# Performance work log

Hardware: AMD Instinct MI355X
Metric: run time of the kernel (lower is better)

Reference implementation:

```python
import jax, jax.numpy as jnp
import numpy as np

N = 50000   # nodes
E = 800000  # edges (avg degree 16)
C = 96      # in = hidden = out channels


def setup_inputs() -> dict:
    key = jax.random.key(0)
    ks = jax.random.split(key, 8)
    s = np.float32(1.0 / np.sqrt(C))
    x = jax.random.normal(ks[0], (N, C), dtype=jnp.float32)
    edge_index = jax.random.randint(ks[1], (2, E), 0, N, dtype=jnp.int64)
    W1 = jax.random.normal(ks[2], (C, C), dtype=jnp.float32) * s
    Wr1 = jax.random.normal(ks[3], (C, C), dtype=jnp.float32) * s
    b1 = jnp.zeros((C,), dtype=jnp.float32)
    W2 = jax.random.normal(ks[4], (C, C), dtype=jnp.float32) * s
    Wr2 = jax.random.normal(ks[5], (C, C), dtype=jnp.float32) * s
    b2 = jnp.zeros((C,), dtype=jnp.float32)
    return {"x": x, "edge_index": edge_index,
            "W1": W1, "Wr1": Wr1, "b1": b1,
            "W2": W2, "Wr2": Wr2, "b2": b2}


def spline_conv(x, edge_index, W, W_root, b):
    """Gather-transform-scatter message passing (SplineConv core, mean aggr)."""
    src, dst = edge_index[0], edge_index[1]
    h = x @ W                                   # [N, C] transform once per node
    msg = h[src]                                # [E, C] edge gather
    agg = jax.ops.segment_sum(msg, dst, num_segments=N)        # scatter-add
    deg = jax.ops.segment_sum(jnp.ones((E,), x.dtype), dst, num_segments=N)
    agg = agg / jnp.maximum(deg, 1.0)[:, None]  # mean aggregation
    return agg + x @ W_root + b                 # root weight + bias


def reference(x, edge_index, W1, Wr1, b1, W2, Wr2, b2):
    h = jax.nn.relu(spline_conv(x, edge_index, W1, Wr1, b1))
    out = spline_conv(h, edge_index, W2, Wr2, b2)
    return out.reshape(-1)  # generalization of x.view(1600)
```

## Files before the change

### kernel.cpp

```cpp
#include <hip/hip_runtime.h>

#define C 96
#define BKT_SHIFT 9
#define BKT_SIZE 512
#define CAP 10240
#define EB 2048
typedef unsigned char u8;
typedef unsigned short u16;
typedef unsigned int u32;
typedef __attribute__((ext_vector_type(8))) short short8;
typedef __attribute__((ext_vector_type(4))) float floatx4;
typedef __attribute__((ext_vector_type(2))) float floatx2;

__device__ inline u16 f2bf(float f) {
    union { float f; u32 u; } v; v.f = f;
    u32 r = v.u + 0x7fff + ((v.u >> 16) & 1);
    return (u16)(r >> 16);
}
__device__ inline u32 pk4_fp8(float a, float b, float c, float d) {
    u32 w = 0;
    w = __builtin_amdgcn_cvt_pk_fp8_f32(a, b, w, false);
    w = __builtin_amdgcn_cvt_pk_fp8_f32(c, d, w, true);
    return w;
}
__device__ inline u8 f2fp8(float a) {
    return (u8)(__builtin_amdgcn_cvt_pk_fp8_f32(a, a, 0, false) & 0xff);
}

__global__ __launch_bounds__(256) void binA_kernel(const int* __restrict__ src,
                                                   const int* __restrict__ dst,
                                                   int* __restrict__ blk_cnt,
                                                   int* __restrict__ blk_off,
                                                   u32* __restrict__ stage, int E) {
    __shared__ u32 s_word[EB];
    __shared__ int s_cnt[128];
    __shared__ int s_inc[128];
    int bid = blockIdx.x;
    int t = threadIdx.x;
    int e0 = bid * EB;
    int cnt_here = min(EB, E - e0);

    for (int i = t; i < 128; i += 256) s_cnt[i] = 0;
    __syncthreads();

    int my_src[EB / 256], my_dl[EB / 256], my_b[EB / 256], my_rank[EB / 256];
    int nmine = 0;
#pragma unroll
    for (int k = 0; k < EB / 256; k++) {
        int i = t + k * 256;
        if (i < cnt_here) {
            int s = src[e0 + i], d = dst[e0 + i];
            int b = d >> BKT_SHIFT;
            my_src[nmine] = s;
            my_dl[nmine] = d & (BKT_SIZE - 1);
            my_b[nmine] = b;
            my_rank[nmine] = atomicAdd(&s_cnt[b], 1);
            nmine++;
        }
    }
    __syncthreads();

    if (t < 128) s_inc[t] = s_cnt[t];
    __syncthreads();
    for (int off = 1; off < 128; off <<= 1) {
        int x2 = (t >= off && t < 128) ? s_inc[t - off] : 0;
        __syncthreads();
        if (t < 128) s_inc[t] += x2;
        __syncthreads();
    }
    if (t < 128) {
        blk_cnt[bid * 128 + t] = s_cnt[t];
        blk_off[bid * 128 + t] = s_inc[t] - s_cnt[t];
    }

    for (int k = 0; k < nmine; k++) {
        int b = my_b[k];
        int slot = (s_inc[b] - s_cnt[b]) + my_rank[k];
        s_word[slot] = ((u32)my_dl[k] << 16) | (u32)my_src[k];
    }
    __syncthreads();

    for (int i = t; i < cnt_here; i += 256) stage[(size_t)bid * EB + i] = s_word[i];
}

__global__ __launch_bounds__(256) void binB_kernel(const u32* __restrict__ stage,
                                                   const int* __restrict__ blk_cnt,
                                                   const int* __restrict__ blk_off,
                                                   int* __restrict__ deg,
                                                   int* __restrict__ row_off,
                                                   u16* __restrict__ csr, int N, int DB,
                                                   int nbkt,
                                                   const float* __restrict__ x,
                                                   u16* __restrict__ xb,
                                                   u8* __restrict__ xf8, int n16, int CX,
                                                   const float* W0, const float* W1,
                                                   const float* W2, const float* W3,
                                                   u16* T0, u16* T1, u16* T2, u16* T3) {
    int bid = blockIdx.x;
    int t = threadIdx.x;
    if (bid >= nbkt) {
        if (bid < nbkt + CX) {
            int i = (bid - nbkt) * 256 + t;
            if (i >= n16) return;
            const float4* p = (const float4*)x + (size_t)i * 4;
            float4 a = p[0], b = p[1], c = p[2], d = p[3];
            short8 o0, o1;
            o0[0] = (short)f2bf(a.x); o0[1] = (short)f2bf(a.y);
            o0[2] = (short)f2bf(a.z); o0[3] = (short)f2bf(a.w);
            o0[4] = (short)f2bf(b.x); o0[5] = (short)f2bf(b.y);
            o0[6] = (short)f2bf(b.z); o0[7] = (short)f2bf(b.w);
            o1[0] = (short)f2bf(c.x); o1[1] = (short)f2bf(c.y);
            o1[2] = (short)f2bf(c.z); o1[3] = (short)f2bf(c.w);
            o1[4] = (short)f2bf(d.x); o1[5] = (short)f2bf(d.y);
            o1[6] = (short)f2bf(d.z); o1[7] = (short)f2bf(d.w);
            *(short8*)(xb + (size_t)i * 16) = o0;
            *(short8*)(xb + (size_t)i * 16 + 8) = o1;
            uint4 f8;
            f8.x = pk4_fp8(a.x, a.y, a.z, a.w);
            f8.y = pk4_fp8(b.x, b.y, b.z, b.w);
            f8.z = pk4_fp8(c.x, c.y, c.z, c.w);
            f8.w = pk4_fp8(d.x, d.y, d.z, d.w);
            *(uint4*)(xf8 + (size_t)i * 16) = f8;
        } else {
            int w = bid - nbkt - CX;
            const float* W = w == 0 ? W0 : w == 1 ? W1 : w == 2 ? W2 : W3;
            u16* T = w == 0 ? T0 : w == 1 ? T1 : w == 2 ? T2 : T3;
            for (int i = t; i < C * C; i += 256) {
                int k = i / C, n = i - k * C;
                T[n * C + k] = f2bf(W[i]);
            }
        }
        return;
    }

    __shared__ int cnt[BKT_SIZE];
    __shared__ int cur[BKT_SIZE];
    __shared__ int ssum[256];
    int b = bid;
    int n0 = b << BKT_SHIFT;
    int nn = min(BKT_SIZE, N - n0);
    int s0 = b * CAP;

    for (int i = t; i < BKT_SIZE; i += 256) cnt[i] = 0;
    __syncthreads();

    for (int i = t; i < DB; i += 256) {
        int len = blk_cnt[i * 128 + b];
        const u32* run = stage + (size_t)i * EB + blk_off[i * 128 + b];
        for (int j = 0; j < len; j++) atomicAdd(&cnt[run[j] >> 16], 1);
    }
    __syncthreads();

    int a0 = cnt[2 * t], a1 = cnt[2 * t + 1];
    ssum[t] = a0 + a1;
    __syncthreads();
    for (int off = 1; off < 256; off <<= 1) {
        int x2 = (t >= off) ? ssum[t - off] : 0;
        __syncthreads();
        ssum[t] += x2;
        __syncthreads();
    }
    int excl = ssum[t] - (a0 + a1);
    if (2 * t < nn) { deg[n0 + 2 * t] = a0; row_off[n0 + 2 * t] = s0 + excl; }
    if (2 * t + 1 < nn) { deg[n0 + 2 * t + 1] = a1; row_off[n0 + 2 * t + 1] = s0 + excl + a0; }
    __syncthreads();
    cur[2 * t] = s0 + excl;
    cur[2 * t + 1] = s0 + excl + a0;
    __syncthreads();

    for (int i = t; i < DB; i += 256) {
        int len = blk_cnt[i * 128 + b];
        const u32* run = stage + (size_t)i * EB + blk_off[i * 128 + b];
        for (int j = 0; j < len; j++) {
            u32 w = run[j];
            int p = atomicAdd(&cur[w >> 16], 1);
            csr[p] = (u16)(w & 0xffffu);
        }
    }
}

template <bool RELU, bool WF8, typename OT>
__global__ __launch_bounds__(256, 4) void layer_kernel(const u16* __restrict__ Xbf,
                                                       const u8* __restrict__ Xf8,
                                                       const int* __restrict__ row_off,
                                                       const int* __restrict__ deg,
                                                       const u16* __restrict__ csr,
                                                       const u16* __restrict__ WTA,
                                                       const u16* __restrict__ WTR,
                                                       const float* __restrict__ BIAS,
                                                       OT* __restrict__ Y,
                                                       u8* __restrict__ Yf8, int n) {
    __shared__ u16 sA[64 * 104];
    __shared__ int s_dg[64];
    __shared__ int s_perm[64];
    const int t = threadIdx.x;
    const int row0 = blockIdx.x * 64;

    if (t < 64) {
        int node = row0 + t;
        s_dg[t] = (node < n) ? deg[node] : 0;
    }
    __syncthreads();
    if (t < 64) {
        int di = s_dg[t];
        int r = 0;
#pragma unroll 8
        for (int j = 0; j < 64; j++) {
            int dj = s_dg[j];
            r += (dj < di) || (dj == di && j < t);
        }
        s_perm[r] = t;
    }
    __syncthreads();

    {
        int nl = s_perm[t >> 2];
        int node = row0 + nl;
        int q = t & 3;
        float acc[24];
#pragma unroll
        for (int i = 0; i < 24; i++) acc[i] = 0.f;
        int d = 0, start = 0;
        if (node < n) { start = row_off[node]; d = s_dg[nl]; }
        const int off4 = q * 16;
        const int off2 = 64 + q * 8;

        int j = 0;
        if (d >= 4) {
            int si[4];
#pragma unroll
            for (int k = 0; k < 4; k++) si[k] = csr[start + k];
            for (; j + 8 <= d; j += 4) {
                uint4 va[4];
                uint2 vb[4];
#pragma unroll
                for (int k = 0; k < 4; k++) {
                    const u8* p = Xf8 + (size_t)si[k] * 96;
                    va[k] = *(const uint4*)(p + off4);
                    vb[k] = *(const uint2*)(p + off2);
                }
                int sn[4];
#pragma unroll
                for (int k = 0; k < 4; k++) sn[k] = csr[start + j + 4 + k];
#pragma unroll
                for (int k = 0; k < 4; k++) {
                    u32 ws[6] = {va[k].x, va[k].y, va[k].z,
                                 va[k].w, vb[k].x, vb[k].y};
#pragma unroll
                    for (int i = 0; i < 6; i++) {
                        floatx2 lo = __builtin_amdgcn_cvt_pk_f32_fp8(ws[i], false);
                        floatx2 hi = __builtin_amdgcn_cvt_pk_f32_fp8(ws[i], true);
                        acc[4 * i]     += lo[0];
                        acc[4 * i + 1] += lo[1];
                        acc[4 * i + 2] += hi[0];
                        acc[4 * i + 3] += hi[1];
                    }
                }
#pragma unroll
                for (int k = 0; k < 4; k++) si[k] = sn[k];
            }
            {
                uint4 va[4];
                uint2 vb[4];
#pragma unroll
                for (int k = 0; k < 4; k++) {
                    const u8* p = Xf8 + (size_t)si[k] * 96;
                    va[k] = *(const uint4*)(p + off4);
                    vb[k] = *(const uint2*)(p + off2);
                }
#pragma unroll
                for (int k = 0; k < 4; k++) {
                    u32 ws[6] = {va[k].x, va[k].y, va[k].z,
                                 va[k].w, vb[k].x, vb[k].y};
#pragma unroll
                    for (int i = 0; i < 6; i++) {
                        floatx2 lo = __builtin_amdgcn_cvt_pk_f32_fp8(ws[i], false);
                        floatx2 hi = __builtin_amdgcn_cvt_pk_f32_fp8(ws[i], true);
                        acc[4 * i]     += lo[0];
                        acc[4 * i + 1] += lo[1];
                        acc[4 * i + 2] += hi[0];
                        acc[4 * i + 3] += hi[1];
                    }
                }
                j += 4;
            }
        }
        for (; j < d; j++) {
            const u8* p = Xf8 + (size_t)csr[start + j] * 96;
            uint4 va = *(const uint4*)(p + off4);
            uint2 vb = *(const uint2*)(p + off2);
            u32 ws[6] = {va.x, va.y, va.z, va.w, vb.x, vb.y};
#pragma unroll
            for (int i = 0; i < 6; i++) {
                floatx2 lo = __builtin_amdgcn_cvt_pk_f32_fp8(ws[i], false);
                floatx2 hi = __builtin_amdgcn_cvt_pk_f32_fp8(ws[i], true);
                acc[4 * i]     += lo[0];
                acc[4 * i + 1] += lo[1];
                acc[4 * i + 2] += hi[0];
                acc[4 * i + 3] += hi[1];
            }
        }
        float inv = 1.0f / fmaxf((float)d, 1.0f);
        u16* dl = sA + nl * 104;
        short8 o0, o1, o2;
#pragma unroll
        for (int i = 0; i < 8; i++) {
            o0[i] = (short)f2bf(acc[i] * inv);
            o1[i] = (short)f2bf(acc[8 + i] * inv);
            o2[i] = (short)f2bf(acc[16 + i] * inv);
        }
        *(short8*)(dl + q * 16) = o0;
        *(short8*)(dl + q * 16 + 8) = o1;
        *(short8*)(dl + 64 + q * 8) = o2;
    }
    __syncthreads();

    const int lane = t & 63;
    const int w = t >> 6;
    const int quad = lane >> 4;
    const int l16 = lane & 15;
    const int r0 = row0 + w * 16;

    floatx4 acc6[6];
#pragma unroll
    for (int i = 0; i < 6; i++) acc6[i] = (floatx4){0.f, 0.f, 0.f, 0.f};

    {
        const u16* Ap = sA + (w * 16 + l16) * 104 + quad * 8;
        const u16* Wp = WTA + l16 * C + quad * 8;
#pragma unroll
        for (int ks = 0; ks < 3; ks++) {
            short8 a = *(const short8*)(Ap + ks * 32);
#pragma unroll
            for (int nt = 0; nt < 6; nt++) {
                short8 b = *(const short8*)(Wp + nt * 16 * C + ks * 32);
                acc6[nt] = __builtin_amdgcn_mfma_f32_16x16x32_bf16(a, b, acc6[nt], 0, 0, 0);
            }
        }
    }
    {
        int arow = r0 + l16;
        if (arow >= n) arow = n - 1;
        const u16* Xp = Xbf + (size_t)arow * C + quad * 8;
        const u16* Wp = WTR + l16 * C + quad * 8;
#pragma unroll
        for (int ks = 0; ks < 3; ks++) {
            short8 a = *(const short8*)(Xp + ks * 32);
#pragma unroll
            for (int nt = 0; nt < 6; nt++) {
                short8 b = *(const short8*)(Wp + nt * 16 * C + ks * 32);
                acc6[nt] = __builtin_amdgcn_mfma_f32_16x16x32_bf16(a, b, acc6[nt], 0, 0, 0);
            }
        }
    }

#pragma unroll
    for (int nt = 0; nt < 6; nt++) {
        float bv = BIAS[nt * 16 + l16];
#pragma unroll
        for (int r = 0; r < 4; r++) {
            float v = acc6[nt][r] + bv;
            if (RELU) v = fmaxf(v, 0.f);
            acc6[nt][r] = v;
        }
    }
    __syncthreads();

    const int nrow = min(64, n - row0);
    const int lr = w * 16 + quad * 4;

    if constexpr (sizeof(OT) == 2) {
        u16* so = sA;
#pragma unroll
        for (int nt = 0; nt < 6; nt++)
#pragma unroll
            for (int r = 0; r < 4; r++)
                so[(lr + r) * 96 + nt * 16 + l16] = f2bf(acc6[nt][r]);
        __syncthreads();
        {
            char* dst = (char*)Y + (size_t)row0 * 192;
            int nbytes = nrow * 192;
            for (int ofs = t * 16; ofs < nbytes; ofs += 4096)
                *(uint4*)(dst + ofs) = *(const uint4*)((const char*)sA + ofs);
        }
        if constexpr (WF8) {
            __syncthreads();
            u8* so8 = (u8*)sA;
#pragma unroll
            for (int nt = 0; nt < 6; nt++)
#pragma unroll
                for (int r = 0; r < 4; r++)
                    so8[(lr + r) * 96 + nt * 16 + l16] = f2fp8(acc6[nt][r]);
            __syncthreads();
            char* dst8 = (char*)Yf8 + (size_t)row0 * 96;
            int nb8 = nrow * 96;
            for (int ofs = t * 16; ofs < nb8; ofs += 4096)
                *(uint4*)(dst8 + ofs) = *(const uint4*)((const char*)sA + ofs);
        }
    } else {
        float* sof = (float*)sA;
#pragma unroll
        for (int half = 0; half < 2; half++) {
            if (half) __syncthreads();
            if ((w >> 1) == half) {
#pragma unroll
                for (int nt = 0; nt < 6; nt++)
#pragma unroll
                    for (int r = 0; r < 4; r++)
                        sof[((w & 1) * 16 + quad * 4 + r) * 96 + nt * 16 + l16] = acc6[nt][r];
            }
            __syncthreads();
            int rbase = row0 + half * 32;
            int nr = n - rbase;
            nr = nr < 0 ? 0 : (nr > 32 ? 32 : nr);
            char* dst = (char*)Y + (size_t)rbase * 384;
            int nbytes = nr * 384;
            for (int ofs = t * 16; ofs < nbytes; ofs += 4096)
                *(uint4*)(dst + ofs) = *(const uint4*)((const char*)sA + ofs);
        }
    }
}

extern "C" void kernel_launch(void* const* d_in, const int* in_sizes, int n_in,
                              void* d_out, int out_size, void* d_ws, size_t ws_size,
                              hipStream_t stream) {
    const float* x   = (const float*)d_in[0];
    const int*   ei  = (const int*)d_in[1];
    const float* W1  = (const float*)d_in[2];
    const float* Wr1 = (const float*)d_in[3];
    const float* b1  = (const float*)d_in[4];
    const float* W2  = (const float*)d_in[5];
    const float* Wr2 = (const float*)d_in[6];
    const float* b2  = (const float*)d_in[7];
    float* out = (float*)d_out;

    const int N = in_sizes[0] / C;
    const int E = in_sizes[1] / 2;
    const int* src = ei;
    const int* dst = ei + E;

    const int nbkt = (N + BKT_SIZE - 1) >> BKT_SHIFT;
    const int DB   = (E + EB - 1) / EB;
    const int n16  = N * C / 16;
    const int CX   = (n16 + 255) / 256;
    int Npad = (N + 63) & ~63;

    int*  blk_cnt = (int*)d_ws;
    int*  blk_off = blk_cnt + DB * 128;
    int*  deg     = blk_off + DB * 128;
    int*  row_off = deg + Npad;
    u32*  stage   = (u32*)(row_off + Npad);
    u16*  csr     = (u16*)(stage + (size_t)DB * EB);
    u16*  xb      = csr + (((size_t)nbkt * CAP + 7) & ~(size_t)7);
    u16*  h1b     = xb + (size_t)N * C;
    u16*  wt      = h1b + (size_t)N * C;
    u16 *wt1 = wt, *wtr1 = wt + C * C, *wt2 = wt + 2 * C * C, *wtr2 = wt + 3 * C * C;
    u8*   xf8     = (u8*)(wt + 4 * C * C);
    u8*   h1f8    = xf8 + (size_t)N * 96;

    const int grid64 = (N + 63) / 64;

    binA_kernel<<<DB, 256, 0, stream>>>(src, dst, blk_cnt, blk_off, stage, E);
    binB_kernel<<<nbkt + CX + 4, 256, 0, stream>>>(stage, blk_cnt, blk_off,
                                                   deg, row_off, csr, N, DB, nbkt,
                                                   x, xb, xf8, n16, CX,
                                                   W1, Wr1, W2, Wr2, wt1, wtr1, wt2, wtr2);

    layer_kernel<true, true, u16><<<grid64, 256, 0, stream>>>(
        xb, xf8, row_off, deg, csr, wt1, wtr1, b1, h1b, h1f8, N);
    layer_kernel<false, false, float><<<grid64, 256, 0, stream>>>(
        h1b, h1f8, row_off, deg, csr, wt2, wtr2, b2, out, h1f8, N);
}
```

Baseline: 164.6 us.

## Bin edges into 64-node tiles and build per-tile CSR inside layer kernels

```diff
diff --git a/kernel.cpp b/kernel.cpp
--- a/kernel.cpp
+++ b/kernel.cpp
@@ -1,10 +1,10 @@
 #include <hip/hip_runtime.h>
 
 #define C 96
-#define BKT_SHIFT 9
-#define BKT_SIZE 512
-#define CAP 10240
+#define TB 64
 #define EB 2048
+#define NBP 1024
+#define LCAP 2048
 typedef unsigned char u8;
 typedef unsigned short u16;
 typedef unsigned int u32;
@@ -27,69 +27,12 @@
     return (u8)(__builtin_amdgcn_cvt_pk_fp8_f32(a, a, 0, false) & 0xff);
 }
 
-__global__ __launch_bounds__(256) void binA_kernel(const int* __restrict__ src,
+__global__ __launch_bounds__(256) void sort_kernel(const int* __restrict__ src,
                                                    const int* __restrict__ dst,
-                                                   int* __restrict__ blk_cnt,
-                                                   int* __restrict__ blk_off,
-                                                   u32* __restrict__ stage, int E) {
-    __shared__ u32 s_word[EB];
-    __shared__ int s_cnt[128];
-    __shared__ int s_inc[128];
-    int bid = blockIdx.x;
-    int t = threadIdx.x;
-    int e0 = bid * EB;
-    int cnt_here = min(EB, E - e0);
-
-    for (int i = t; i < 128; i += 256) s_cnt[i] = 0;
-    __syncthreads();
-
-    int my_src[EB / 256], my_dl[EB / 256], my_b[EB / 256], my_rank[EB / 256];
-    int nmine = 0;
-#pragma unroll
-    for (int k = 0; k < EB / 256; k++) {
-        int i = t + k * 256;
-        if (i < cnt_here) {
-            int s = src[e0 + i], d = dst[e0 + i];
-            int b = d >> BKT_SHIFT;
-            my_src[nmine] = s;
-            my_dl[nmine] = d & (BKT_SIZE - 1);
-            my_b[nmine] = b;
-            my_rank[nmine] = atomicAdd(&s_cnt[b], 1);
-            nmine++;
-        }
-    }
-    __syncthreads();
-
-    if (t < 128) s_inc[t] = s_cnt[t];
-    __syncthreads();
-    for (int off = 1; off < 128; off <<= 1) {
-        int x2 = (t >= off && t < 128) ? s_inc[t - off] : 0;
-        __syncthreads();
-        if (t < 128) s_inc[t] += x2;
-        __syncthreads();
-    }
-    if (t < 128) {
-        blk_cnt[bid * 128 + t] = s_cnt[t];
-        blk_off[bid * 128 + t] = s_inc[t] - s_cnt[t];
-    }
-
-    for (int k = 0; k < nmine; k++) {
-        int b = my_b[k];
-        int slot = (s_inc[b] - s_cnt[b]) + my_rank[k];
-        s_word[slot] = ((u32)my_dl[k] << 16) | (u32)my_src[k];
-    }
-    __syncthreads();
-
-    for (int i = t; i < cnt_here; i += 256) stage[(size_t)bid * EB + i] = s_word[i];
-}
-
-__global__ __launch_bounds__(256) void binB_kernel(const u32* __restrict__ stage,
-                                                   const int* __restrict__ blk_cnt,
-                                                   const int* __restrict__ blk_off,
-                                                   int* __restrict__ deg,
-                                                   int* __restrict__ row_off,
-                                                   u16* __restrict__ csr, int N, int DB,
-                                                   int nbkt,
+                                                   int* __restrict__ cntT,
+                                                   int* __restrict__ offT,
+                                                   u32* __restrict__ stage,
+                                                   int E, int DB, int NB,
                                                    const float* __restrict__ x,
                                                    u16* __restrict__ xb,
                                                    u8* __restrict__ xf8, int n16, int CX,
@@ -98,9 +41,10 @@
                                                    u16* T0, u16* T1, u16* T2, u16* T3) {
     int bid = blockIdx.x;
     int t = threadIdx.x;
-    if (bid >= nbkt) {
-        if (bid < nbkt + CX) {
-            int i = (bid - nbkt) * 256 + t;
+    if (bid >= DB) {
+        int cc = bid - DB;
+        if (cc < CX) {
+            int i = cc * 256 + t;
             if (i >= n16) return;
             const float4* p = (const float4*)x + (size_t)i * 4;
             float4 a = p[0], b = p[1], c = p[2], d = p[3];
@@ -122,7 +66,7 @@
             f8.w = pk4_fp8(d.x, d.y, d.z, d.w);
             *(uint4*)(xf8 + (size_t)i * 16) = f8;
         } else {
-            int w = bid - nbkt - CX;
+            int w = cc - CX;
             const float* W = w == 0 ? W0 : w == 1 ? W1 : w == 2 ? W2 : W3;
             u16* T = w == 0 ? T0 : w == 1 ? T1 : w == 2 ? T2 : T3;
             for (int i = t; i < C * C; i += 256) {
@@ -133,80 +77,131 @@
         return;
     }
 
-    __shared__ int cnt[BKT_SIZE];
-    __shared__ int cur[BKT_SIZE];
-    __shared__ int ssum[256];
-    int b = bid;
-    int n0 = b << BKT_SHIFT;
-    int nn = min(BKT_SIZE, N - n0);
-    int s0 = b * CAP;
-
-    for (int i = t; i < BKT_SIZE; i += 256) cnt[i] = 0;
-    __syncthreads();
-
-    for (int i = t; i < DB; i += 256) {
-        int len = blk_cnt[i * 128 + b];
-        const u32* run = stage + (size_t)i * EB + blk_off[i * 128 + b];
-        for (int j = 0; j < len; j++) atomicAdd(&cnt[run[j] >> 16], 1);
-    }
-    __syncthreads();
-
-    int a0 = cnt[2 * t], a1 = cnt[2 * t + 1];
-    ssum[t] = a0 + a1;
+    __shared__ u32 s_word[EB];
+    __shared__ int s_cnt[NBP];
+    __shared__ int s_off[NBP];
+    __shared__ int s_scan[256];
+    int e0 = bid * EB;
+    int cnt_here = min(EB, E - e0);
+
+    for (int i = t; i < NBP; i += 256) s_cnt[i] = 0;
+    __syncthreads();
+
+    int my_src[EB / 256], my_dl[EB / 256], my_b[EB / 256], my_rank[EB / 256];
+    int nmine = 0;
+#pragma unroll
+    for (int k = 0; k < EB / 256; k++) {
+        int i = t + k * 256;
+        if (i < cnt_here) {
+            int s = src[e0 + i], d = dst[e0 + i];
+            int b = d >> 6;
+            my_src[nmine] = s;
+            my_dl[nmine] = d & (TB - 1);
+            my_b[nmine] = b;
+            my_rank[nmine] = atomicAdd(&s_cnt[b], 1);
+            nmine++;
+        }
+    }
+    __syncthreads();
+
+    int b4 = t * 4;
+    int v0 = s_cnt[b4], v1 = s_cnt[b4 + 1], v2 = s_cnt[b4 + 2], v3 = s_cnt[b4 + 3];
+    int lsum = v0 + v1 + v2 + v3;
+    s_scan[t] = lsum;
     __syncthreads();
     for (int off = 1; off < 256; off <<= 1) {
-        int x2 = (t >= off) ? ssum[t - off] : 0;
+        int x2 = (t >= off) ? s_scan[t - off] : 0;
         __syncthreads();
-        ssum[t] += x2;
+        s_scan[t] += x2;
         __syncthreads();
     }
-    int excl = ssum[t] - (a0 + a1);
-    if (2 * t < nn) { deg[n0 + 2 * t] = a0; row_off[n0 + 2 * t] = s0 + excl; }
-    if (2 * t + 1 < nn) { deg[n0 + 2 * t + 1] = a1; row_off[n0 + 2 * t + 1] = s0 + excl + a0; }
-    __syncthreads();
-    cur[2 * t] = s0 + excl;
-    cur[2 * t + 1] = s0 + excl + a0;
-    __syncthreads();
-
-    for (int i = t; i < DB; i += 256) {
-        int len = blk_cnt[i * 128 + b];
-        const u32* run = stage + (size_t)i * EB + blk_off[i * 128 + b];
-        for (int j = 0; j < len; j++) {
-            u32 w = run[j];
-            int p = atomicAdd(&cur[w >> 16], 1);
-            csr[p] = (u16)(w & 0xffffu);
-        }
-    }
+    int excl = s_scan[t] - lsum;
+    s_off[b4] = excl;
+    s_off[b4 + 1] = excl + v0;
+    s_off[b4 + 2] = excl + v0 + v1;
+    s_off[b4 + 3] = excl + v0 + v1 + v2;
+    __syncthreads();
+
+    for (int b = t; b < NB; b += 256) {
+        cntT[(size_t)b * DB + bid] = s_cnt[b];
+        offT[(size_t)b * DB + bid] = s_off[b];
+    }
+
+    for (int k = 0; k < nmine; k++) {
+        int slot = s_off[my_b[k]] + my_rank[k];
+        s_word[slot] = ((u32)my_dl[k] << 16) | (u32)my_src[k];
+    }
+    __syncthreads();
+
+    for (int i = t; i < cnt_here; i += 256) stage[(size_t)bid * EB + i] = s_word[i];
 }
 
 template <bool RELU, bool WF8, typename OT>
 __global__ __launch_bounds__(256, 4) void layer_kernel(const u16* __restrict__ Xbf,
                                                        const u8* __restrict__ Xf8,
-                                                       const int* __restrict__ row_off,
-                                                       const int* __restrict__ deg,
-                                                       const u16* __restrict__ csr,
+                                                       const int* __restrict__ cntT,
+                                                       const int* __restrict__ offT,
+                                                       const u32* __restrict__ stage,
                                                        const u16* __restrict__ WTA,
                                                        const u16* __restrict__ WTR,
                                                        const float* __restrict__ BIAS,
                                                        OT* __restrict__ Y,
-                                                       u8* __restrict__ Yf8, int n) {
-    __shared__ u16 sA[64 * 104];
-    __shared__ int s_dg[64];
-    __shared__ int s_perm[64];
+                                                       u8* __restrict__ Yf8, int n, int DB) {
+    __shared__ __align__(16) u16 sA[64 * 104];
+    __shared__ u16 lcsr[LCAP];
+    __shared__ int s_cnt64[TB];
+    __shared__ int s_off64[TB];
+    __shared__ int s_cur64[TB];
+    __shared__ int s_perm[TB];
     const int t = threadIdx.x;
-    const int row0 = blockIdx.x * 64;
+    const int b = blockIdx.x;
+    const int row0 = b * 64;
+    const int* cntT_b = cntT + (size_t)b * DB;
+    const int* offT_b = offT + (size_t)b * DB;
+
+    for (int i = t; i < TB; i += 256) s_cnt64[i] = 0;
+    __syncthreads();
+    for (int i = t; i < DB; i += 256) {
+        int len = cntT_b[i];
+        const u32* run = stage + (size_t)i * EB + offT_b[i];
+        for (int j = 0; j < len; j++) atomicAdd(&s_cnt64[run[j] >> 16], 1);
+    }
+    __syncthreads();
+
+    int dv = (t < TB) ? s_cnt64[t] : 0;
+    if (t < TB) s_cur64[t] = dv;
+    __syncthreads();
+    for (int off = 1; off < TB; off <<= 1) {
+        int x2 = (t >= off && t < TB) ? s_cur64[t - off] : 0;
+        __syncthreads();
+        if (t < TB) s_cur64[t] += x2;
+        __syncthreads();
+    }
+    if (t < TB) {
+        int excl = s_cur64[t] - dv;
+        s_off64[t] = excl;
+    }
+    __syncthreads();
+    if (t < TB) s_cur64[t] = s_off64[t];
+    __syncthreads();
+
+    for (int i = t; i < DB; i += 256) {
+        int len = cntT_b[i];
+        const u32* run = stage + (size_t)i * EB + offT_b[i];
+        for (int j = 0; j < len; j++) {
+            u32 w = run[j];
+            int p = atomicAdd(&s_cur64[w >> 16], 1);
+            lcsr[p] = (u16)(w & 0xffffu);
+        }
+    }
+    __syncthreads();
 
     if (t < 64) {
-        int node = row0 + t;
-        s_dg[t] = (node < n) ? deg[node] : 0;
-    }
-    __syncthreads();
-    if (t < 64) {
-        int di = s_dg[t];
+        int di = s_cnt64[t];
         int r = 0;
 #pragma unroll 8
         for (int j = 0; j < 64; j++) {
-            int dj = s_dg[j];
+            int dj = s_cnt64[j];
             r += (dj < di) || (dj == di && j < t);
         }
         s_perm[r] = t;
@@ -215,13 +210,12 @@
 
     {
         int nl = s_perm[t >> 2];
-        int node = row0 + nl;
         int q = t & 3;
         float acc[24];
 #pragma unroll
         for (int i = 0; i < 24; i++) acc[i] = 0.f;
-        int d = 0, start = 0;
-        if (node < n) { start = row_off[node]; d = s_dg[nl]; }
+        int d = s_cnt64[nl];
+        int start = s_off64[nl];
         const int off4 = q * 16;
         const int off2 = 64 + q * 8;
 
@@ -229,7 +223,7 @@
         if (d >= 4) {
             int si[4];
 #pragma unroll
-            for (int k = 0; k < 4; k++) si[k] = csr[start + k];
+            for (int k = 0; k < 4; k++) si[k] = lcsr[start + k];
             for (; j + 8 <= d; j += 4) {
                 uint4 va[4];
                 uint2 vb[4];
@@ -241,7 +235,7 @@
                 }
                 int sn[4];
 #pragma unroll
-                for (int k = 0; k < 4; k++) sn[k] = csr[start + j + 4 + k];
+                for (int k = 0; k < 4; k++) sn[k] = lcsr[start + j + 4 + k];
 #pragma unroll
                 for (int k = 0; k < 4; k++) {
                     u32 ws[6] = {va[k].x, va[k].y, va[k].z,
@@ -286,7 +280,7 @@
             }
         }
         for (; j < d; j++) {
-            const u8* p = Xf8 + (size_t)csr[start + j] * 96;
+            const u8* p = Xf8 + (size_t)lcsr[start + j] * 96;
             uint4 va = *(const uint4*)(p + off4);
             uint2 vb = *(const uint2*)(p + off2);
             u32 ws[6] = {va.x, va.y, va.z, va.w, vb.x, vb.y};
@@ -333,8 +327,8 @@
             short8 a = *(const short8*)(Ap + ks * 32);
 #pragma unroll
             for (int nt = 0; nt < 6; nt++) {
-                short8 b = *(const short8*)(Wp + nt * 16 * C + ks * 32);
-                acc6[nt] = __builtin_amdgcn_mfma_f32_16x16x32_bf16(a, b, acc6[nt], 0, 0, 0);
+                short8 bb = *(const short8*)(Wp + nt * 16 * C + ks * 32);
+                acc6[nt] = __builtin_amdgcn_mfma_f32_16x16x32_bf16(a, bb, acc6[nt], 0, 0, 0);
             }
         }
     }
@@ -348,8 +342,8 @@
             short8 a = *(const short8*)(Xp + ks * 32);
 #pragma unroll
             for (int nt = 0; nt < 6; nt++) {
-                short8 b = *(const short8*)(Wp + nt * 16 * C + ks * 32);
-                acc6[nt] = __builtin_amdgcn_mfma_f32_16x16x32_bf16(a, b, acc6[nt], 0, 0, 0);
+                short8 bb = *(const short8*)(Wp + nt * 16 * C + ks * 32);
+                acc6[nt] = __builtin_amdgcn_mfma_f32_16x16x32_bf16(a, bb, acc6[nt], 0, 0, 0);
             }
         }
     }
@@ -378,10 +372,10 @@
                 so[(lr + r) * 96 + nt * 16 + l16] = f2bf(acc6[nt][r]);
         __syncthreads();
         {
-            char* dst = (char*)Y + (size_t)row0 * 192;
+            char* dstp = (char*)Y + (size_t)row0 * 192;
             int nbytes = nrow * 192;
             for (int ofs = t * 16; ofs < nbytes; ofs += 4096)
-                *(uint4*)(dst + ofs) = *(const uint4*)((const char*)sA + ofs);
+                *(uint4*)(dstp + ofs) = *(const uint4*)((const char*)sA + ofs);
         }
         if constexpr (WF8) {
             __syncthreads();
@@ -413,10 +407,10 @@
             int rbase = row0 + half * 32;
             int nr = n - rbase;
             nr = nr < 0 ? 0 : (nr > 32 ? 32 : nr);
-            char* dst = (char*)Y + (size_t)rbase * 384;
+            char* dstp = (char*)Y + (size_t)rbase * 384;
             int nbytes = nr * 384;
             for (int ofs = t * 16; ofs < nbytes; ofs += 4096)
-                *(uint4*)(dst + ofs) = *(const uint4*)((const char*)sA + ofs);
+                *(uint4*)(dstp + ofs) = *(const uint4*)((const char*)sA + ofs);
         }
     }
 }
@@ -439,35 +433,29 @@
     const int* src = ei;
     const int* dst = ei + E;
 
-    const int nbkt = (N + BKT_SIZE - 1) >> BKT_SHIFT;
     const int DB   = (E + EB - 1) / EB;
+    const int NB   = (N + TB - 1) / TB;
     const int n16  = N * C / 16;
     const int CX   = (n16 + 255) / 256;
-    int Npad = (N + 63) & ~63;
-
-    int*  blk_cnt = (int*)d_ws;
-    int*  blk_off = blk_cnt + DB * 128;
-    int*  deg     = blk_off + DB * 128;
-    int*  row_off = deg + Npad;
-    u32*  stage   = (u32*)(row_off + Npad);
-    u16*  csr     = (u16*)(stage + (size_t)DB * EB);
-    u16*  xb      = csr + (((size_t)nbkt * CAP + 7) & ~(size_t)7);
-    u16*  h1b     = xb + (size_t)N * C;
-    u16*  wt      = h1b + (size_t)N * C;
+    const size_t NBDB = ((size_t)NB * DB + 3) & ~(size_t)3;
+
+    int*  cntT = (int*)d_ws;
+    int*  offT = cntT + NBDB;
+    u32*  stage = (u32*)(offT + NBDB);
+    u16*  xb   = (u16*)(stage + (size_t)DB * EB);
+    u16*  h1b  = xb + (size_t)N * C;
+    u16*  wt   = h1b + (size_t)N * C;
     u16 *wt1 = wt, *wtr1 = wt + C * C, *wt2 = wt + 2 * C * C, *wtr2 = wt + 3 * C * C;
-    u8*   xf8     = (u8*)(wt + 4 * C * C);
-    u8*   h1f8    = xf8 + (size_t)N * 96;
-
-    const int grid64 = (N + 63) / 64;
-
-    binA_kernel<<<DB, 256, 0, stream>>>(src, dst, blk_cnt, blk_off, stage, E);
-    binB_kernel<<<nbkt + CX + 4, 256, 0, stream>>>(stage, blk_cnt, blk_off,
-                                                   deg, row_off, csr, N, DB, nbkt,
-                                                   x, xb, xf8, n16, CX,
-                                                   W1, Wr1, W2, Wr2, wt1, wtr1, wt2, wtr2);
-
-    layer_kernel<true, true, u16><<<grid64, 256, 0, stream>>>(
-        xb, xf8, row_off, deg, csr, wt1, wtr1, b1, h1b, h1f8, N);
-    layer_kernel<false, false, float><<<grid64, 256, 0, stream>>>(
-        h1b, h1f8, row_off, deg, csr, wt2, wtr2, b2, out, h1f8, N);
-}
+    u8*   xf8  = (u8*)(wt + 4 * C * C);
+    u8*   h1f8 = xf8 + (size_t)N * 96;
+
+    sort_kernel<<<DB + CX + 4, 256, 0, stream>>>(src, dst, cntT, offT, stage,
+                                                 E, DB, NB,
+                                                 x, xb, xf8, n16, CX,
+                                                 W1, Wr1, W2, Wr2, wt1, wtr1, wt2, wtr2);
+
+    layer_kernel<true, true, u16><<<NB, 256, 0, stream>>>(
+        xb, xf8, cntT, offT, stage, wt1, wtr1, b1, h1b, h1f8, N, DB);
+    layer_kernel<false, false, float><<<NB, 256, 0, stream>>>(
+        h1b, h1f8, cntT, offT, stage, wt2, wtr2, b2, out, h1f8, N, DB);
+}
```

Result: slower. 169.5 us (+3.0%).
